# Performance work log

Hardware: AMD Instinct MI355X
Metric: run time of the kernel (lower is better)

## Reference

```python
import jax, jax.numpy as jnp
import numpy as np

N = 100000
E = 1600000
C_IN = 128
C_OUT = 128


def setup_inputs() -> dict:
    key = jax.random.key(0)
    k1, k2, k3 = jax.random.split(key, 3)
    x = jax.random.normal(k1, (N, C_IN), dtype=jnp.float32)
    edge_index = jax.random.randint(k2, (2, E), 0, N, dtype=jnp.int64)
    # Linear(in, out, bias=False).weight has shape [out, in]
    W = jax.random.normal(k3, (C_OUT, C_IN), dtype=jnp.float32) * (1.0 / np.sqrt(C_IN))
    return {"x": x, "edge_index": edge_index, "W": W}


def reference(x, edge_index, W):
    n_nodes = x.shape[0]
    row, col = edge_index[0], edge_index[1]
    # degree counts only out-edges of row (matches torch `degree(edge_index, N)`)
    deg = jax.ops.segment_sum(jnp.ones((row.shape[0],), dtype=x.dtype), row,
                              num_segments=n_nodes)
    # D_tilde = D + I  ->  normalization n = (deg + 1)^(-1/2)
    inv_sqrt = jax.lax.rsqrt(deg + 1.0)  # [N]
    xs = x * inv_sqrt[:, None]
    # x <- (A + I) x : gather sources (col), scatter-add to destinations (row),
    # plus identity (self) contribution
    agg = jax.ops.segment_sum(xs[col], row, num_segments=n_nodes) + xs
    out = agg * inv_sqrt[:, None]
    # x <- x W^T
    return jnp.matmul(out, W.T)
```

## Files before the change

kernel.cpp:

```cpp
#include <hip/hip_runtime.h>
#include <hip/hip_fp16.h>
#include <math.h>

#define C 128
#define BSHIFT 9
#define BWIDTH 512
#define NBMAX 256
#define COLBITS 17
#define P2CHUNK 4096
#define P3CAP 10240
#define CAP 9216
#define APITCH 136

typedef _Float16 v8hf __attribute__((ext_vector_type(8)));
typedef float v4f __attribute__((ext_vector_type(4)));

__global__ __launch_bounds__(256) void init_wconv_kernel(int* __restrict__ gcur, int NB,
                                                         const float4* __restrict__ W4,
                                                         __half2* __restrict__ Wh2,
                                                         int total4) {
    int t = threadIdx.x;
    if (blockIdx.x == 0) {
        if (t < NB) gcur[t] = t * CAP;
    } else {
        int i = (blockIdx.x - 1) * 256 + t;
        if (i < total4) {
            float4 v = W4[i];
            Wh2[i * 2]     = __floats2half2_rn(v.x, v.y);
            Wh2[i * 2 + 1] = __floats2half2_rn(v.z, v.w);
        }
    }
}

__global__ __launch_bounds__(256) void p2_scatter_kernel(const int* __restrict__ rowI,
                                                         const int* __restrict__ colI,
                                                         int* __restrict__ gcur,
                                                         unsigned* __restrict__ ebuf, int E,
                                                         const float4* __restrict__ x4,
                                                         __half2* __restrict__ xh2, int N) {
    __shared__ int cnt[NBMAX];
    __shared__ int sc[NBMAX];
    __shared__ int delta[NBMAX];
    __shared__ unsigned sorted[P2CHUNK];
    __shared__ unsigned char bkt[P2CHUNK];
    const int t = threadIdx.x;
    cnt[t] = 0;
    __syncthreads();
    const int e0 = blockIdx.x * P2CHUNK;
    int ranks[16];
#pragma unroll
    for (int k = 0; k < 16; ++k) {
        int e = e0 + k * 256 + t;
        if (e < E) ranks[k] = atomicAdd(&cnt[rowI[e] >> BSHIFT], 1);
    }
    __syncthreads();
    sc[t] = cnt[t];
    __syncthreads();
    for (int o = 1; o < 256; o <<= 1) {
        int v = (t >= o) ? sc[t - o] : 0;
        __syncthreads();
        sc[t] += v;
        __syncthreads();
    }
    {
        int c = cnt[t];
        int ls = sc[t] - c;
        int gb = c ? atomicAdd(&gcur[t], c) : 0;
        delta[t] = gb - ls;
        sc[t] = ls;
    }
    __syncthreads();
#pragma unroll
    for (int k = 0; k < 16; ++k) {
        int e = e0 + k * 256 + t;
        if (e < E) {
            int r = rowI[e];
            unsigned cc = (unsigned)colI[e];
            int b = r >> BSHIFT;
            int lp = sc[b] + ranks[k];
            sorted[lp] = ((unsigned)(r & (BWIDTH - 1)) << COLBITS) | cc;
            bkt[lp] = (unsigned char)b;
        }
    }
    __syncthreads();
    int total = E - e0; if (total > P2CHUNK) total = P2CHUNK;
#pragma unroll
    for (int k = 0; k < 16; ++k) {
        int i = k * 256 + t;
        if (i < total) ebuf[delta[bkt[i]] + i] = sorted[i];
    }

    int totalX4 = N * 32;
    for (int i = blockIdx.x * 256 + t; i < totalX4; i += gridDim.x * 256) {
        float4 v = x4[i];
        xh2[i * 2]     = __floats2half2_rn(v.x, v.y);
        xh2[i * 2 + 1] = __floats2half2_rn(v.z, v.w);
    }
}

__global__ __launch_bounds__(512) void p3_place_kernel(const unsigned* __restrict__ ebuf,
                                                       const int* __restrict__ gcur,
                                                       int* __restrict__ offs_start,
                                                       int* __restrict__ offs_end,
                                                       float* __restrict__ inv,
                                                       int* __restrict__ csr, int N) {
    __shared__ int cnt[BWIDTH];
    __shared__ int sc[BWIDTH];
    __shared__ int sortedCol[P3CAP];
    const int b = blockIdx.x;
    const int t = threadIdx.x;
    const int rowBase = b << BSHIFT;
    const int eS = b * CAP;
    const int eE = gcur[b];

    cnt[t] = 0;
    __syncthreads();
    for (int j = eS + t; j < eE; j += 512)
        atomicAdd(&cnt[ebuf[j] >> COLBITS], 1);
    __syncthreads();
    sc[t] = cnt[t];
    __syncthreads();
    for (int o = 1; o < 512; o <<= 1) {
        int v = (t >= o) ? sc[t - o] : 0;
        __syncthreads();
        sc[t] += v;
        __syncthreads();
    }
    int node = rowBase + t;
    int myCnt = cnt[t];
    if (node < N) {
        offs_start[node] = eS + sc[t] - myCnt;
        offs_end[node]   = eS + sc[t];
        inv[node] = rsqrtf((float)myCnt + 1.0f);
    }
    __syncthreads();
    cnt[t] = sc[t] - myCnt;
    __syncthreads();
    for (int j = eS + t; j < eE; j += 512) {
        unsigned rc = ebuf[j];
        int slot = atomicAdd(&cnt[rc >> COLBITS], 1);
        int col = (int)(rc & ((1u << COLBITS) - 1));
        if (slot < P3CAP) sortedCol[slot] = col;
        else csr[eS + slot] = col;
    }
    __syncthreads();
    int total = eE - eS; if (total > P3CAP) total = P3CAP;
    for (int i = t; i < total; i += 512)
        csr[eS + i] = sortedCol[i];
}

#define ACC4F(vv, sI)                                              \
    {                                                              \
        const __half2* p_ = (const __half2*)&(vv);                 \
        _Pragma("unroll")                                          \
        for (int q = 0; q < 4; ++q) {                              \
            float2 f_ = __half22float2(p_[q]);                     \
            a[2 * q]     = fmaf(f_.x, (sI), a[2 * q]);             \
            a[2 * q + 1] = fmaf(f_.y, (sI), a[2 * q + 1]);         \
        }                                                          \
    }

__global__ __launch_bounds__(256) void gather_mm_kernel(const float4* __restrict__ xh4,
                                                        const int* __restrict__ offs_start,
                                                        const int* __restrict__ offs_end,
                                                        const int* __restrict__ csr,
                                                        const float* __restrict__ inv,
                                                        const _Float16* __restrict__ Wh,
                                                        float* __restrict__ out, int N) {
    __shared__ _Float16 agg[16][APITCH];
    const int tid = threadIdx.x;
    const int base = blockIdx.x * 16;
    const int r = tid >> 4;
    const int c16 = tid & 15;
    const int node = base + r;

    float a[8] = {0, 0, 0, 0, 0, 0, 0, 0};
    float invn = 0.0f;
    if (node < N) {
        int s = offs_start[node];
        int e = offs_end[node];
        invn = inv[node];
        {
            float4 h = xh4[(size_t)node * 16 + c16];
            ACC4F(h, invn)
        }
        int j = s;
        for (; j + 4 <= e; j += 4) {
            int c0 = csr[j], c1 = csr[j + 1], c2 = csr[j + 2], c3 = csr[j + 3];
            float i0 = inv[c0], i1 = inv[c1], i2 = inv[c2], i3 = inv[c3];
            float4 v0 = xh4[(size_t)c0 * 16 + c16];
            float4 v1 = xh4[(size_t)c1 * 16 + c16];
            float4 v2 = xh4[(size_t)c2 * 16 + c16];
            float4 v3 = xh4[(size_t)c3 * 16 + c16];
            ACC4F(v0, i0) ACC4F(v1, i1) ACC4F(v2, i2) ACC4F(v3, i3)
        }
        for (; j < e; ++j) {
            int c = csr[j];
            float ic = inv[c];
            float4 v = xh4[(size_t)c * 16 + c16];
            ACC4F(v, ic)
        }
#pragma unroll
        for (int q = 0; q < 8; ++q) a[q] *= invn;
    }
    {
        __half2 hh[4];
#pragma unroll
        for (int q = 0; q < 4; ++q) hh[q] = __floats2half2_rn(a[2 * q], a[2 * q + 1]);
        *(float4*)&agg[r][c16 * 8] = *(const float4*)hh;
    }
    __syncthreads();

    const int wave = tid >> 6;
    const int lane = tid & 63;
    const int rr = lane & 15;
    const int kg = lane >> 4;

    v8hf av[4];
#pragma unroll
    for (int kk = 0; kk < 4; ++kk)
        av[kk] = *(const v8hf*)&agg[rr][kg * 8 + kk * 32];

#pragma unroll
    for (int ti = 0; ti < 2; ++ti) {
        const int t = wave * 2 + ti;
        v4f acc = {0.0f, 0.0f, 0.0f, 0.0f};
        const v8hf* bp = (const v8hf*)(Wh + (size_t)(t * 16 + rr) * C + kg * 8);
#pragma unroll
        for (int kk = 0; kk < 4; ++kk)
            acc = __builtin_amdgcn_mfma_f32_16x16x32_f16(av[kk], bp[kk * 4], acc, 0, 0, 0);
#pragma unroll
        for (int reg = 0; reg < 4; ++reg) {
            int orow = base + kg * 4 + reg;
            if (orow < N) out[(size_t)orow * C + t * 16 + rr] = acc[reg];
        }
    }
}

extern "C" void kernel_launch(void* const* d_in, const int* in_sizes, int n_in,
                              void* d_out, int out_size, void* d_ws, size_t ws_size,
                              hipStream_t stream) {
    const float* x  = (const float*)d_in[0];
    const int*   ei = (const int*)d_in[1];
    const float* W  = (const float*)d_in[2];
    float* out = (float*)d_out;

    const int N = in_sizes[0] / C;
    const int E = in_sizes[1] / 2;
    const int* rowI = ei;
    const int* colI = ei + E;

    const int NB = (N + BWIDTH - 1) / BWIDTH;

    char* ws = (char*)d_ws;
    size_t off = 0;
    auto carve = [&](size_t bytes) -> void* {
        off = (off + 255) & ~(size_t)255;
        void* p = ws + off;
        off += bytes;
        return p;
    };
    int*      gcur       = (int*)carve((size_t)NBMAX * 4);
    int*      offs_start = (int*)carve((size_t)N * 4);
    int*      offs_end   = (int*)carve((size_t)N * 4);
    float*    inv        = (float*)carve((size_t)N * 4);
    int*      csr        = (int*)carve((size_t)NB * CAP * 4);
    __half2*  xh         = (__half2*)carve((size_t)N * C * 2);
    unsigned* ebuf       = (unsigned*)carve((size_t)NB * CAP * 4);
    __half2*  Wh         = (__half2*)carve((size_t)C * C * 2);

    int wtotal4 = C * C / 4;
    init_wconv_kernel<<<1 + (wtotal4 + 255) / 256, 256, 0, stream>>>(
        gcur, NB, (const float4*)W, Wh, wtotal4);

    int nChunks = (E + P2CHUNK - 1) / P2CHUNK;
    p2_scatter_kernel<<<nChunks, 256, 0, stream>>>(rowI, colI, gcur, ebuf, E,
                                                   (const float4*)x, xh, N);
    p3_place_kernel<<<NB, 512, 0, stream>>>(ebuf, gcur, offs_start, offs_end, inv, csr, N);

    gather_mm_kernel<<<(N + 15) / 16, 256, 0, stream>>>((const float4*)xh, offs_start,
                                                        offs_end, csr, inv,
                                                        (const _Float16*)Wh, out, N);
}
```

Before: 129.3 us.

## Gather directly into MFMA register layout, removing shared-memory staging per wave

Each wave now owns 16 nodes. Every lane gathers the four k-slices of one node's row, laid out to match the MFMA A-operand, so the aggregated values go straight into registers without an LDS round trip or block barrier. Each wave computes all 8 output tiles itself, and the grid shrinks to 64 nodes per block. The cost is that each lane handles 4x more loads per edge with a shallower edge unroll. Register pressure rises with 32 accumulators, and lanes of the same row issue scattered 16-byte loads instead of one contiguous row per 16 lanes.

```diff
diff --git a/kernel.cpp b/kernel.cpp
--- a/kernel.cpp
+++ b/kernel.cpp
@@ -10,7 +10,6 @@
 #define P2CHUNK 4096
 #define P3CAP 10240
 #define CAP 9216
-#define APITCH 136
 
 typedef _Float16 v8hf __attribute__((ext_vector_type(8)));
 typedef float v4f __attribute__((ext_vector_type(4)));
@@ -149,14 +148,14 @@
         csr[eS + i] = sortedCol[i];
 }
 
-#define ACC4F(vv, sI)                                              \
+#define ACCC(kk, vv, sI)                                           \
     {                                                              \
         const __half2* p_ = (const __half2*)&(vv);                 \
         _Pragma("unroll")                                          \
         for (int q = 0; q < 4; ++q) {                              \
             float2 f_ = __half22float2(p_[q]);                     \
-            a[2 * q]     = fmaf(f_.x, (sI), a[2 * q]);             \
-            a[2 * q + 1] = fmaf(f_.y, (sI), a[2 * q + 1]);         \
+            a[kk][2 * q]     = fmaf(f_.x, (sI), a[kk][2 * q]);     \
+            a[kk][2 * q + 1] = fmaf(f_.y, (sI), a[kk][2 * q + 1]); \
         }                                                          \
     }
 
@@ -167,72 +166,75 @@
                                                         const float* __restrict__ inv,
                                                         const _Float16* __restrict__ Wh,
                                                         float* __restrict__ out, int N) {
-    __shared__ _Float16 agg[16][APITCH];
     const int tid = threadIdx.x;
-    const int base = blockIdx.x * 16;
-    const int r = tid >> 4;
-    const int c16 = tid & 15;
+    const int wv = tid >> 6;
+    const int lane = tid & 63;
+    const int r = lane & 15;
+    const int kg = lane >> 4;
+    const int base = blockIdx.x * 64 + wv * 16;
+    if (base >= N) return;
     const int node = base + r;
 
-    float a[8] = {0, 0, 0, 0, 0, 0, 0, 0};
-    float invn = 0.0f;
+    float a[4][8];
+#pragma unroll
+    for (int kk = 0; kk < 4; ++kk)
+#pragma unroll
+        for (int q = 0; q < 8; ++q) a[kk][q] = 0.0f;
+
     if (node < N) {
-        int s = offs_start[node];
-        int e = offs_end[node];
-        invn = inv[node];
+        const int s = offs_start[node];
+        const int e = offs_end[node];
+        const float invn = inv[node];
         {
-            float4 h = xh4[(size_t)node * 16 + c16];
-            ACC4F(h, invn)
+            const float4* rp = xh4 + (size_t)node * 16;
+            float4 h0 = rp[kg], h1 = rp[kg + 4], h2 = rp[kg + 8], h3 = rp[kg + 12];
+            ACCC(0, h0, invn) ACCC(1, h1, invn) ACCC(2, h2, invn) ACCC(3, h3, invn)
         }
         int j = s;
-        for (; j + 4 <= e; j += 4) {
-            int c0 = csr[j], c1 = csr[j + 1], c2 = csr[j + 2], c3 = csr[j + 3];
-            float i0 = inv[c0], i1 = inv[c1], i2 = inv[c2], i3 = inv[c3];
-            float4 v0 = xh4[(size_t)c0 * 16 + c16];
-            float4 v1 = xh4[(size_t)c1 * 16 + c16];
-            float4 v2 = xh4[(size_t)c2 * 16 + c16];
-            float4 v3 = xh4[(size_t)c3 * 16 + c16];
-            ACC4F(v0, i0) ACC4F(v1, i1) ACC4F(v2, i2) ACC4F(v3, i3)
-        }
-        for (; j < e; ++j) {
+        for (; j + 2 <= e; j += 2) {
+            int c0 = csr[j], c1 = csr[j + 1];
+            float i0 = inv[c0], i1 = inv[c1];
+            const float4* p0 = xh4 + (size_t)c0 * 16;
+            const float4* p1 = xh4 + (size_t)c1 * 16;
+            float4 u0 = p0[kg], u1 = p0[kg + 4], u2 = p0[kg + 8], u3 = p0[kg + 12];
+            float4 w0 = p1[kg], w1 = p1[kg + 4], w2 = p1[kg + 8], w3 = p1[kg + 12];
+            ACCC(0, u0, i0) ACCC(1, u1, i0) ACCC(2, u2, i0) ACCC(3, u3, i0)
+            ACCC(0, w0, i1) ACCC(1, w1, i1) ACCC(2, w2, i1) ACCC(3, w3, i1)
+        }
+        if (j < e) {
             int c = csr[j];
             float ic = inv[c];
-            float4 v = xh4[(size_t)c * 16 + c16];
-            ACC4F(v, ic)
-        }
-#pragma unroll
-        for (int q = 0; q < 8; ++q) a[q] *= invn;
-    }
-    {
+            const float4* p = xh4 + (size_t)c * 16;
+            float4 u0 = p[kg], u1 = p[kg + 4], u2 = p[kg + 8], u3 = p[kg + 12];
+            ACCC(0, u0, ic) ACCC(1, u1, ic) ACCC(2, u2, ic) ACCC(3, u3, ic)
+        }
+#pragma unroll
+        for (int kk = 0; kk < 4; ++kk)
+#pragma unroll
+            for (int q = 0; q < 8; ++q) a[kk][q] *= invn;
+    }
+
+    v8hf av[4];
+#pragma unroll
+    for (int kk = 0; kk < 4; ++kk) {
         __half2 hh[4];
 #pragma unroll
-        for (int q = 0; q < 4; ++q) hh[q] = __floats2half2_rn(a[2 * q], a[2 * q + 1]);
-        *(float4*)&agg[r][c16 * 8] = *(const float4*)hh;
-    }
-    __syncthreads();
-
-    const int wave = tid >> 6;
-    const int lane = tid & 63;
-    const int rr = lane & 15;
-    const int kg = lane >> 4;
-
-    v8hf av[4];
-#pragma unroll
-    for (int kk = 0; kk < 4; ++kk)
-        av[kk] = *(const v8hf*)&agg[rr][kg * 8 + kk * 32];
-
-#pragma unroll
-    for (int ti = 0; ti < 2; ++ti) {
-        const int t = wave * 2 + ti;
+        for (int q = 0; q < 4; ++q)
+            hh[q] = __floats2half2_rn(a[kk][2 * q], a[kk][2 * q + 1]);
+        av[kk] = *(const v8hf*)hh;
+    }
+
+#pragma unroll
+    for (int t = 0; t < 8; ++t) {
         v4f acc = {0.0f, 0.0f, 0.0f, 0.0f};
-        const v8hf* bp = (const v8hf*)(Wh + (size_t)(t * 16 + rr) * C + kg * 8);
+        const v8hf* bp = (const v8hf*)(Wh + (size_t)(t * 16 + r) * C + kg * 8);
 #pragma unroll
         for (int kk = 0; kk < 4; ++kk)
             acc = __builtin_amdgcn_mfma_f32_16x16x32_f16(av[kk], bp[kk * 4], acc, 0, 0, 0);
 #pragma unroll
         for (int reg = 0; reg < 4; ++reg) {
             int orow = base + kg * 4 + reg;
-            if (orow < N) out[(size_t)orow * C + t * 16 + rr] = acc[reg];
+            if (orow < N) out[(size_t)orow * C + t * 16 + r] = acc[reg];
         }
     }
 }
@@ -278,7 +280,7 @@
                                                    (const float4*)x, xh, N);
     p3_place_kernel<<<NB, 512, 0, stream>>>(ebuf, gcur, offs_start, offs_end, inv, csr, N);
 
-    gather_mm_kernel<<<(N + 15) / 16, 256, 0, stream>>>((const float4*)xh, offs_start,
+    gather_mm_kernel<<<(N + 63) / 64, 256, 0, stream>>>((const float4*)xh, offs_start,
                                                         offs_end, csr, inv,
                                                         (const _Float16*)Wh, out, N);
 }
```

After: 149.7 us. 1.16x slower.
